# Kernel optimization log

Hardware: AMD Instinct MI355X
Metric: run time of the kernel (lower is better)

## Reference

```python
import jax, jax.numpy as jnp
import numpy as np

B, M, N = 262144, 3, 256   # batch, soil layers, runoff features
H1, H2 = 256, 128          # MLP hidden widths (layer_units[:-1]); last layer is scalar


def setup_inputs() -> dict:
    key = jax.random.key(0)
    ks = jax.random.split(key, 9)
    runoff = jax.random.uniform(ks[0], (B, M, N), dtype=jnp.float32)
    last_flow = jax.random.uniform(ks[1], (B, M), dtype=jnp.float32)
    last_free_water = jax.random.uniform(ks[2], (B, M), dtype=jnp.float32)
    s = 0.05
    # m independent tiny MLPs, stacked along leading axis m
    W1 = jax.random.normal(ks[3], (M, N, H1), dtype=jnp.float32) * s
    b1 = jnp.zeros((M, H1), dtype=jnp.float32)
    W2 = jax.random.normal(ks[4], (M, H1, H2), dtype=jnp.float32) * s
    b2 = jnp.zeros((M, H2), dtype=jnp.float32)
    W3 = jax.random.normal(ks[5], (M, H2), dtype=jnp.float32) * s  # last layer has 1 unit
    b3 = jnp.zeros((M,), dtype=jnp.float32)
    return {
        "last_flow": last_flow,
        "last_free_water": last_free_water,
        "runoff": runoff,
        "W1": W1, "b1": b1, "W2": W2, "b2": b2, "W3": W3, "b3": b3,
    }


def reference(last_flow, last_free_water, runoff, W1, b1, W2, b2, W3, b3):
    # step 1: add summed runoff to free-water state  (B, M)
    free_water = last_free_water + jnp.sum(runoff, axis=-1)
    # step 2: m small MLPs -> per-layer outflow ratio in (0,1), batched over m via einsum
    a1 = jax.nn.relu(jnp.einsum('bmn,mnh->bmh', runoff, W1) + b1)        # (B, M, H1)
    a2 = jax.nn.relu(jnp.einsum('bmh,mhk->bmk', a1, W2) + b2)            # (B, M, H2)
    ratio = jax.nn.sigmoid(jnp.einsum('bmk,mk->bm', a2, W3) + b3)        # (B, M)
    # step 3: blend free water with previous flow
    flow = free_water * ratio + last_flow * (1.0 - ratio)
    # step 4: update free-water state
    new_free_water = free_water - flow
    return (new_free_water, flow)
```

## Files before the change

### kernel.cpp

```cpp
#include <hip/hip_runtime.h>
#include <hip/hip_bf16.h>


#define B_TOT 262144
#define M_    3
#define N_    256
#define H1_   256
#define H2_   128
#define BM_   (B_TOT * M_)

typedef __bf16 bf16_t;
typedef __bf16  bf16x8 __attribute__((ext_vector_type(8)));
typedef float   f32x16 __attribute__((ext_vector_type(16)));
typedef float   f32x4  __attribute__((ext_vector_type(4)));

__device__ __forceinline__ unsigned pack_bf2(float lo, float hi) {
  union { bf16_t b; unsigned short u; } a, c;
  a.b = (bf16_t)lo; c.b = (bf16_t)hi;
  return ((unsigned)c.u << 16) | (unsigned)a.u;
}

__device__ __forceinline__ void gload_lds16(const void* g, void* l) {
  __builtin_amdgcn_global_load_lds(
      (const __attribute__((address_space(1))) void*)g,
      (__attribute__((address_space(3))) void*)l, 16, 0, 0);
}

__global__ __launch_bounds__(256) void prep_weights(
    const float* __restrict__ W1, const float* __restrict__ W2,
    bf16_t* __restrict__ w1s, bf16_t* __restrict__ w2s)
{
  int id = blockIdx.x * 256 + threadIdx.x;
  const int NW1 = M_ * 16 * 8 * 64;
  const int NW2 = M_ * 16 * 4 * 64;
  if (id < NW1) {
    int lane = id & 63;
    int t    = (id >> 6) & 7;
    int kk   = (id >> 9) & 15;
    int m    = id >> 13;
    int h  = 32 * t + (lane & 31);
    int n0 = 16 * kk + 8 * (lane >> 5);
    bf16x8 v;
#pragma unroll
    for (int ii = 0; ii < 8; ++ii)
      v[ii] = (bf16_t)W1[((size_t)m * N_ + (n0 + ii)) * H1_ + h];
    *reinterpret_cast<bf16x8*>(&w1s[(size_t)id * 8]) = v;
  } else if (id < NW1 + NW2) {
    int j    = id - NW1;
    int lane = j & 63;
    int t2   = (j >> 6) & 3;
    int kk2  = (j >> 8) & 15;
    int m    = j >> 12;
    int k2 = 32 * t2 + (lane & 31);
    int h0 = 16 * kk2 + 8 * (lane >> 5);
    bf16x8 v;
#pragma unroll
    for (int ii = 0; ii < 8; ++ii)
      v[ii] = (bf16_t)W2[((size_t)m * H1_ + (h0 + ii)) * H2_ + k2];
    *reinterpret_cast<bf16x8*>(&w2s[(size_t)j * 8]) = v;
  }
}

__global__ __launch_bounds__(256, 1) void reservoir_kernel(
    const float* __restrict__ last_flow,
    const float* __restrict__ last_fw,
    const float* __restrict__ runoff,
    const float* __restrict__ b1,
    const float* __restrict__ b2,
    const float* __restrict__ W3,
    const float* __restrict__ b3,
    const bf16_t* __restrict__ w1s,
    const bf16_t* __restrict__ w2s,
    float* __restrict__ out)
{
  __shared__ alignas(16) float  sR[3][128 * 32];
  __shared__ alignas(16) bf16_t sW1[2][8192];
  __shared__ alignas(16) bf16_t sW2[16 * 2048];
  __shared__ alignas(16) float  sB1[H1_];
  __shared__ alignas(16) float  sB2[H2_];
  __shared__ alignas(16) float  sW3[H2_];

  const int tid  = threadIdx.x;
  const int lane = tid & 63;
  const int wv   = tid >> 6;
  const int hi   = lane >> 5;
  const int r    = lane & 31;
  const int r7   = r & 7;
  const int l3   = lane >> 3;
  const int gsw  = (lane & 7) ^ l3;

  const int bidx  = blockIdx.x;
  const int m     = bidx >> 8;
  const int rbase = (bidx & 255) * 1024;

  const bf16_t* w1base = w1s + (size_t)m * 65536;
  const bf16_t* w2base = w2s + (size_t)m * 32768;

  auto stage_R = [&](int ai) {
    int aic  = ai < 63 ? ai : 63;
    int row0 = rbase + (aic >> 3) * 128;
    int g    = aic & 7;
    float* dst = &sR[ai % 3][0];
#pragma unroll
    for (int c = 0; c < 4; ++c) {
      int slab = wv * 4 + c;
      const float* src = runoff
          + ((size_t)(row0 + slab * 8 + l3) * M_ + m) * N_ + 32 * g + 4 * gsw;
      gload_lds16(src, dst + slab * 256);
    }
  };
  auto stage_W1 = [&](int wai) {
    int g = wai & 7;
    bf16_t* dst = &sW1[wai & 1][0];
#pragma unroll
    for (int c = 0; c < 4; ++c) {
      int chunk = wv * 4 + c;
      gload_lds16(w1base + (size_t)g * 8192 + chunk * 512 + lane * 8,
                  dst + chunk * 512);
    }
  };

  stage_R(0);  stage_W1(0);
  stage_R(1);  stage_W1(1);
  stage_R(2);
#pragma unroll
  for (int i = 0; i < 16; ++i) {
    int chunk = wv * 16 + i;
    gload_lds16(w2base + (size_t)chunk * 512 + lane * 8, &sW2[chunk * 512]);
  }
  sB1[tid] = b1[m * H1_ + tid];
  if (tid < H2_) { sB2[tid] = b2[m * H2_ + tid]; sW3[tid] = W3[m * H2_ + tid]; }
  __syncthreads();

  for (int u = 0; u < 8; ++u) {
    const int row = rbase + u * 128 + wv * 32 + r;

    f32x16 acc1[8];
#pragma unroll
    for (int t = 0; t < 8; ++t) {
#pragma unroll
      for (int g2 = 0; g2 < 4; ++g2) {
        f32x4 bv = *reinterpret_cast<const f32x4*>(&sB1[32 * t + 8 * g2 + 4 * hi]);
        acc1[t][4 * g2 + 0] = bv[0];
        acc1[t][4 * g2 + 1] = bv[1];
        acc1[t][4 * g2 + 2] = bv[2];
        acc1[t][4 * g2 + 3] = bv[3];
      }
    }
    float rsum = 0.f;

    for (int g = 0; g < 8; ++g) {
      const int ai = u * 8 + g;
      asm volatile("s_waitcnt vmcnt(8)" ::: "memory");
      __builtin_amdgcn_sched_barrier(0);
      __builtin_amdgcn_s_barrier();

      const float*  rp = &sR[ai % 3][(wv * 32 + r) * 32];
      const bf16_t* wp = &sW1[ai & 1][0];
#pragma unroll
      for (int q = 0; q < 2; ++q) {
        f32x4 qa = *reinterpret_cast<const f32x4*>(&rp[((4 * q + 2 * hi + 0) ^ r7) * 4]);
        f32x4 qb = *reinterpret_cast<const f32x4*>(&rp[((4 * q + 2 * hi + 1) ^ r7) * 4]);
        rsum += qa[0] + qa[1] + qa[2] + qa[3] + qb[0] + qb[1] + qb[2] + qb[3];
        bf16x8 bfrag;
        bfrag[0] = (bf16_t)qa[0]; bfrag[1] = (bf16_t)qa[1];
        bfrag[2] = (bf16_t)qa[2]; bfrag[3] = (bf16_t)qa[3];
        bfrag[4] = (bf16_t)qb[0]; bfrag[5] = (bf16_t)qb[1];
        bfrag[6] = (bf16_t)qb[2]; bfrag[7] = (bf16_t)qb[3];
#pragma unroll
        for (int t = 0; t < 8; ++t) {
          bf16x8 afrag = *reinterpret_cast<const bf16x8*>(
              &wp[q * 4096 + t * 512 + lane * 8]);
          acc1[t] = __builtin_amdgcn_mfma_f32_32x32x16_bf16(afrag, bfrag, acc1[t], 0, 0, 0);
        }
      }

      __builtin_amdgcn_s_barrier();
      stage_R(ai + 3);
      stage_W1(ai + 2);
    }

    unsigned P[8][2][2][2];
#pragma unroll
    for (int t = 0; t < 8; ++t)
#pragma unroll
      for (int q = 0; q < 2; ++q)
#pragma unroll
        for (int v = 0; v < 2; ++v)
#pragma unroll
          for (int s = 0; s < 2; ++s) {
            int e = 8 * q + 4 * v + 2 * s;
            P[t][q][v][s] = pack_bf2(fmaxf(acc1[t][e], 0.f),
                                     fmaxf(acc1[t][e + 1], 0.f));
          }

    f32x16 acc2[4];
#pragma unroll
    for (int t2 = 0; t2 < 4; ++t2) {
#pragma unroll
      for (int g2 = 0; g2 < 4; ++g2) {
        f32x4 bv = *reinterpret_cast<const f32x4*>(&sB2[32 * t2 + 8 * g2 + 4 * hi]);
        acc2[t2][4 * g2 + 0] = bv[0];
        acc2[t2][4 * g2 + 1] = bv[1];
        acc2[t2][4 * g2 + 2] = bv[2];
        acc2[t2][4 * g2 + 3] = bv[3];
      }
    }

#pragma unroll
    for (int kk2 = 0; kk2 < 16; ++kk2) {
      const int t = kk2 >> 1, q = kk2 & 1;
      auto r0 = __builtin_amdgcn_permlane32_swap(P[t][q][0][0], P[t][q][1][0], false, false);
      auto r1 = __builtin_amdgcn_permlane32_swap(P[t][q][0][1], P[t][q][1][1], false, false);
      union { unsigned uu[4]; bf16x8 v; } bb;
      bb.uu[0] = r0[0]; bb.uu[1] = r1[0]; bb.uu[2] = r0[1]; bb.uu[3] = r1[1];
#pragma unroll
      for (int t2 = 0; t2 < 4; ++t2) {
        bf16x8 afrag = *reinterpret_cast<const bf16x8*>(
            &sW2[kk2 * 2048 + t2 * 512 + lane * 8]);
        acc2[t2] = __builtin_amdgcn_mfma_f32_32x32x16_bf16(afrag, bb.v, acc2[t2], 0, 0, 0);
      }
    }

    float part = 0.f;
#pragma unroll
    for (int t2 = 0; t2 < 4; ++t2) {
#pragma unroll
      for (int g2 = 0; g2 < 4; ++g2) {
        f32x4 w3v = *reinterpret_cast<const f32x4*>(&sW3[32 * t2 + 8 * g2 + 4 * hi]);
        part += fmaxf(acc2[t2][4 * g2 + 0], 0.f) * w3v[0]
              + fmaxf(acc2[t2][4 * g2 + 1], 0.f) * w3v[1]
              + fmaxf(acc2[t2][4 * g2 + 2], 0.f) * w3v[2]
              + fmaxf(acc2[t2][4 * g2 + 3], 0.f) * w3v[3];
      }
    }
    part += __shfl_xor(part, 32, 64);
    rsum += __shfl_xor(rsum, 32, 64);

    const float x     = part + b3[m];
    const float ratio = 1.0f / (1.0f + __expf(-x));
    const size_t oi   = (size_t)row * M_ + m;
    const float fw    = last_fw[oi] + rsum;
    const float lf    = last_flow[oi];
    const float flow  = fw * ratio + lf * (1.0f - ratio);
    if (hi == 0) {
      out[oi]        = fw - flow;
      out[BM_ + oi]  = flow;
    }
  }
}

extern "C" void kernel_launch(void* const* d_in, const int* in_sizes, int n_in,
                              void* d_out, int out_size, void* d_ws, size_t ws_size,
                              hipStream_t stream) {
  const float* last_flow = (const float*)d_in[0];
  const float* last_fw   = (const float*)d_in[1];
  const float* runoff    = (const float*)d_in[2];
  const float* W1 = (const float*)d_in[3];
  const float* b1 = (const float*)d_in[4];
  const float* W2 = (const float*)d_in[5];
  const float* b2 = (const float*)d_in[6];
  const float* W3 = (const float*)d_in[7];
  const float* b3 = (const float*)d_in[8];
  float* out = (float*)d_out;

  bf16_t* w1s = (bf16_t*)d_ws;
  bf16_t* w2s = w1s + (size_t)M_ * 65536;

  prep_weights<<<144, 256, 0, stream>>>(W1, W2, w1s, w2s);

  reservoir_kernel<<<768, 256, 0, stream>>>(last_flow, last_fw, runoff,
                                            b1, b2, W3, b3, w1s, w2s, out);
}
```

Before: 284.9 us.

## Prefetch runoff into registers, store as bf16 per-wave LDS tile, triple-buffer W1

Runoff rows are loaded directly into registers for the next 128-row tile while the current tile's MLP runs. They are then converted to bf16 and written to a swizzled per-wave LDS buffer, which replaces the fp32 async global-to-LDS staging. W1 is streamed in smaller 16-deep K slices with a three-slot ring, and block indices are remapped to interleave layers and chunks. This is meant to halve LDS footprint and traffic for runoff and overlap global loads with compute. It costs more registers, and the runoff sum is now taken over bf16-rounded values, which reduces precision.

```diff
diff --git a/kernel.cpp b/kernel.cpp
--- a/kernel.cpp
+++ b/kernel.cpp
@@ -73,9 +73,9 @@
     const bf16_t* __restrict__ w2s,
     float* __restrict__ out)
 {
-  __shared__ alignas(16) float  sR[3][128 * 32];
-  __shared__ alignas(16) bf16_t sW1[2][8192];
-  __shared__ alignas(16) bf16_t sW2[16 * 2048];
+  __shared__ alignas(16) bf16_t sRb[4][8192];
+  __shared__ alignas(16) bf16_t sW1[3][4096];
+  __shared__ alignas(16) bf16_t sW2[32768];
   __shared__ alignas(16) float  sB1[H1_];
   __shared__ alignas(16) float  sB2[H2_];
   __shared__ alignas(16) float  sW3[H2_];
@@ -85,55 +85,60 @@
   const int wv   = tid >> 6;
   const int hi   = lane >> 5;
   const int r    = lane & 31;
-  const int r7   = r & 7;
-  const int l3   = lane >> 3;
-  const int gsw  = (lane & 7) ^ l3;
-
-  const int bidx  = blockIdx.x;
-  const int m     = bidx >> 8;
-  const int rbase = (bidx & 255) * 1024;
+
+  const int x     = blockIdx.x & 7;
+  const int s     = blockIdx.x >> 3;
+  const int m     = s % 3;
+  const int chunk = x * 32 + s / 3;
+  const size_t rbase = (size_t)chunk * 1024;
 
   const bf16_t* w1base = w1s + (size_t)m * 65536;
   const bf16_t* w2base = w2s + (size_t)m * 32768;
 
-  auto stage_R = [&](int ai) {
-    int aic  = ai < 63 ? ai : 63;
-    int row0 = rbase + (aic >> 3) * 128;
-    int g    = aic & 7;
-    float* dst = &sR[ai % 3][0];
-#pragma unroll
-    for (int c = 0; c < 4; ++c) {
-      int slab = wv * 4 + c;
-      const float* src = runoff
-          + ((size_t)(row0 + slab * 8 + l3) * M_ + m) * N_ + 32 * g + 4 * gsw;
-      gload_lds16(src, dst + slab * 256);
+  auto stage_w1 = [&](int gkn) {
+    int kkp = gkn & 15;
+    int sl  = gkn % 3;
+#pragma unroll
+    for (int c = 0; c < 2; ++c) {
+      int chk = wv * 2 + c;
+      gload_lds16(w1base + (size_t)kkp * 4096 + chk * 512 + lane * 8,
+                  &sW1[sl][chk * 512]);
     }
   };
-  auto stage_W1 = [&](int wai) {
-    int g = wai & 7;
-    bf16_t* dst = &sW1[wai & 1][0];
-#pragma unroll
-    for (int c = 0; c < 4; ++c) {
-      int chunk = wv * 4 + c;
-      gload_lds16(w1base + (size_t)g * 8192 + chunk * 512 + lane * 8,
-                  dst + chunk * 512);
-    }
+
+  f32x4 rbuf[32];
+  auto issue_R = [&](int u) {
+    const float* base = runoff
+        + (((size_t)(rbase + u * 128 + wv * 32)) * M_ + m) * N_ + lane * 4;
+#pragma unroll
+    for (int i = 0; i < 32; ++i)
+      rbuf[i] = *reinterpret_cast<const f32x4*>(base + (size_t)i * (M_ * N_));
+    __builtin_amdgcn_sched_barrier(0);
   };
 
-  stage_R(0);  stage_W1(0);
-  stage_R(1);  stage_W1(1);
-  stage_R(2);
+  issue_R(0);
+  stage_w1(0);
 #pragma unroll
   for (int i = 0; i < 16; ++i) {
-    int chunk = wv * 16 + i;
-    gload_lds16(w2base + (size_t)chunk * 512 + lane * 8, &sW2[chunk * 512]);
+    int chk = wv * 16 + i;
+    gload_lds16(w2base + (size_t)chk * 512 + lane * 8, &sW2[chk * 512]);
   }
   sB1[tid] = b1[m * H1_ + tid];
   if (tid < H2_) { sB2[tid] = b2[m * H2_ + tid]; sW3[tid] = W3[m * H2_ + tid]; }
-  __syncthreads();
 
   for (int u = 0; u < 8; ++u) {
-    const int row = rbase + u * 128 + wv * 32 + r;
+    const int row = (int)rbase + u * 128 + wv * 32 + r;
+
+    asm volatile("s_waitcnt vmcnt(0) lgkmcnt(0)" ::: "memory");
+    __builtin_amdgcn_s_barrier();
+#pragma unroll
+    for (int i = 0; i < 32; ++i) {
+      uint2 dd;
+      dd.x = pack_bf2(rbuf[i][0], rbuf[i][1]);
+      dd.y = pack_bf2(rbuf[i][2], rbuf[i][3]);
+      int p8 = lane ^ ((i & 15) << 1);
+      *reinterpret_cast<uint2*>(&sRb[wv][i * 256 + p8 * 4]) = dd;
+    }
 
     f32x16 acc1[8];
 #pragma unroll
@@ -149,36 +154,32 @@
     }
     float rsum = 0.f;
 
-    for (int g = 0; g < 8; ++g) {
-      const int ai = u * 8 + g;
-      asm volatile("s_waitcnt vmcnt(8)" ::: "memory");
+#pragma unroll
+    for (int kk = 0; kk < 16; ++kk) {
+      const int gk = u * 16 + kk;
+      if (u < 7 || kk < 15) {
+        stage_w1(gk + 1);
+        asm volatile("s_waitcnt vmcnt(2)" ::: "memory");
+      } else {
+        asm volatile("s_waitcnt vmcnt(0)" ::: "memory");
+      }
       __builtin_amdgcn_sched_barrier(0);
       __builtin_amdgcn_s_barrier();
 
-      const float*  rp = &sR[ai % 3][(wv * 32 + r) * 32];
-      const bf16_t* wp = &sW1[ai & 1][0];
-#pragma unroll
-      for (int q = 0; q < 2; ++q) {
-        f32x4 qa = *reinterpret_cast<const f32x4*>(&rp[((4 * q + 2 * hi + 0) ^ r7) * 4]);
-        f32x4 qb = *reinterpret_cast<const f32x4*>(&rp[((4 * q + 2 * hi + 1) ^ r7) * 4]);
-        rsum += qa[0] + qa[1] + qa[2] + qa[3] + qb[0] + qb[1] + qb[2] + qb[3];
-        bf16x8 bfrag;
-        bfrag[0] = (bf16_t)qa[0]; bfrag[1] = (bf16_t)qa[1];
-        bfrag[2] = (bf16_t)qa[2]; bfrag[3] = (bf16_t)qa[3];
-        bfrag[4] = (bf16_t)qb[0]; bfrag[5] = (bf16_t)qb[1];
-        bfrag[6] = (bf16_t)qb[2]; bfrag[7] = (bf16_t)qb[3];
-#pragma unroll
-        for (int t = 0; t < 8; ++t) {
-          bf16x8 afrag = *reinterpret_cast<const bf16x8*>(
-              &wp[q * 4096 + t * 512 + lane * 8]);
-          acc1[t] = __builtin_amdgcn_mfma_f32_32x32x16_bf16(afrag, bfrag, acc1[t], 0, 0, 0);
-        }
-      }
-
-      __builtin_amdgcn_s_barrier();
-      stage_R(ai + 3);
-      stage_W1(ai + 2);
-    }
+      const int sl = gk % 3;
+      bf16x8 bfrag = *reinterpret_cast<const bf16x8*>(
+          &sRb[wv][r * 256 + (((2 * kk + hi) ^ (r & 15)) * 8)]);
+#pragma unroll
+      for (int j = 0; j < 8; ++j) rsum += (float)bfrag[j];
+#pragma unroll
+      for (int t = 0; t < 8; ++t) {
+        bf16x8 afrag = *reinterpret_cast<const bf16x8*>(
+            &sW1[sl][t * 512 + lane * 8]);
+        acc1[t] = __builtin_amdgcn_mfma_f32_32x32x16_bf16(afrag, bfrag, acc1[t], 0, 0, 0);
+      }
+    }
+
+    if (u < 7) issue_R(u + 1);
 
     unsigned P[8][2][2][2];
 #pragma unroll
@@ -188,10 +189,10 @@
 #pragma unroll
         for (int v = 0; v < 2; ++v)
 #pragma unroll
-          for (int s = 0; s < 2; ++s) {
-            int e = 8 * q + 4 * v + 2 * s;
-            P[t][q][v][s] = pack_bf2(fmaxf(acc1[t][e], 0.f),
-                                     fmaxf(acc1[t][e + 1], 0.f));
+          for (int ss = 0; ss < 2; ++ss) {
+            int e = 8 * q + 4 * v + 2 * ss;
+            P[t][q][v][ss] = pack_bf2(fmaxf(acc1[t][e], 0.f),
+                                      fmaxf(acc1[t][e + 1], 0.f));
           }
 
     f32x16 acc2[4];
@@ -237,8 +238,8 @@
     part += __shfl_xor(part, 32, 64);
     rsum += __shfl_xor(rsum, 32, 64);
 
-    const float x     = part + b3[m];
-    const float ratio = 1.0f / (1.0f + __expf(-x));
+    const float xx    = part + b3[m];
+    const float ratio = 1.0f / (1.0f + __expf(-xx));
     const size_t oi   = (size_t)row * M_ + m;
     const float fw    = last_fw[oi] + rsum;
     const float lf    = last_flow[oi];
```

Measured after the change: 491.6 us. +72.6%, slower.
